# Kernel tuning notes

Hardware: AMD Instinct MI355X
Metric: run time of the kernel (lower is better)

## Reference

```python
import jax, jax.numpy as jnp
import numpy as np

# Mamba2 config fixed by MambaIndexer.__init__: d_state=64, expand=1, headdim=32
D_MODEL = 1024
D_STATE = 64
EXPAND = 1
D_INNER = EXPAND * D_MODEL          # 1024
HEADDIM = 32
NHEADS = D_INNER // HEADDIM         # 32
D_CONV = 4
NGROUPS = 1
IDX_DIM = 64
SEQ = 2048
CONV_DIM = D_INNER + 2 * NGROUPS * D_STATE            # 1152 (x, B, C share the conv)
D_IN_PROJ = 2 * D_INNER + 2 * NGROUPS * D_STATE + NHEADS  # 2208 (z, xBC, dt)


def setup_inputs() -> dict:
    key = jax.random.key(0)
    ks = jax.random.split(key, 10)
    s = 0.02  # init scale for projection weights
    return {
        "x": jax.random.normal(ks[0], (SEQ, D_MODEL), jnp.float32),
        "W_in": jax.random.normal(ks[1], (D_MODEL, D_IN_PROJ), jnp.float32) * s,
        "conv_w": jax.random.normal(ks[2], (CONV_DIM, D_CONV), jnp.float32) * s,
        "conv_b": jnp.zeros((CONV_DIM,), jnp.float32),
        "dt_bias": jax.random.normal(ks[3], (NHEADS,), jnp.float32) * 0.1,
        "A_log": jax.random.uniform(ks[4], (NHEADS,), jnp.float32, 0.0, 1.5),
        "D": jax.random.normal(ks[5], (NHEADS,), jnp.float32),
        "norm_w": jnp.ones((D_INNER,), jnp.float32),
        "W_out": jax.random.normal(ks[6], (D_INNER, D_MODEL), jnp.float32) * s,
        "Wq": jax.random.normal(ks[7], (D_MODEL, IDX_DIM), jnp.float32) * s,
        "Wk": jax.random.normal(ks[8], (D_MODEL, IDX_DIM), jnp.float32) * s,
    }


def _mamba2(x, W_in, conv_w, conv_b, dt_bias, A_log, D, norm_w, W_out):
    L = x.shape[0]
    zxbcdt = x @ W_in                                   # (L, 2208)
    z = zxbcdt[:, :D_INNER]                             # gate
    xBC = zxbcdt[:, D_INNER:D_INNER + CONV_DIM]
    dt = jax.nn.softplus(zxbcdt[:, D_INNER + CONV_DIM:] + dt_bias)  # (L, H)
    # causal depthwise conv1d over seq, kernel 4, then silu
    conv = jax.lax.conv_general_dilated(
        xBC.T[None],                                    # (1, C, L)
        conv_w[:, None, :],                             # (C, 1, K)
        (1,), [(D_CONV - 1, 0)], feature_group_count=CONV_DIM)
    xBC = jax.nn.silu(conv[0].T + conv_b)               # (L, C)
    xs = xBC[:, :D_INNER].reshape(L, NHEADS, HEADDIM)   # (L, H, P)
    B = xBC[:, D_INNER:D_INNER + D_STATE]               # (L, N), ngroups=1
    C = xBC[:, D_INNER + D_STATE:]                      # (L, N)
    A = -jnp.exp(A_log)                                 # (H,)
    dA = jnp.exp(dt * A)                                # (L, H)
    dBx = jnp.einsum('lh,lhp,ln->lhpn', dt, xs, B)      # (L, H, P, N)

    def step(h, inp):
        dA_t, dBx_t, C_t = inp
        h = dA_t[:, None, None] * h + dBx_t             # (H, P, N)
        return h, jnp.einsum('hpn,n->hp', h, C_t)

    h0 = jnp.zeros((NHEADS, HEADDIM, D_STATE), x.dtype)
    _, y = jax.lax.scan(step, h0, (dA, dBx, C))         # y: (L, H, P)
    y = y + D[:, None] * xs                             # skip connection
    y = y.reshape(L, D_INNER) * jax.nn.silu(z)          # gated
    y = y * jax.lax.rsqrt(jnp.mean(y * y, axis=-1, keepdims=True) + 1e-5) * norm_w
    return y @ W_out                                    # (L, d_model)


def reference(x, W_in, conv_w, conv_b, dt_bias, A_log, D, norm_w, W_out, Wq, Wk):
    L = x.shape[0]
    x_mamba = _mamba2(x, W_in, conv_w, conv_b, dt_bias, A_log, D, norm_w, W_out)
    q = x_mamba @ Wq                                    # (L, idx)
    k = x @ Wk                                          # (L, idx)
    scores = jnp.einsum('ti,si->ts', q, k) * (IDX_DIM ** -0.5)
    mask = jnp.tril(jnp.ones((L, L), dtype=bool))
    return jnp.where(mask, scores, -jnp.inf)
```

## Files before the change

### kernel.cpp

```cpp
#include <hip/hip_runtime.h>
#include <hip/hip_bf16.h>
#include <math.h>
#include <float.h>

#define SEQ 2048
#define DMODEL 1024
#define DINNER 1024
#define DSTATE 64
#define HEADDIM 32
#define NHEADS 32
#define DCONV 4
#define CONVDIM 1152
#define DINPROJ 2208
#define DINPROJ_PAD 2304
#define IDXDIM 64

#define CHUNK 64
#define NCHUNKS (SEQ / CHUNK)

#define MASK_VAL (-1e30f)

typedef unsigned short u16;
typedef __bf16 bf16x8 __attribute__((ext_vector_type(8)));
typedef float f32x4 __attribute__((ext_vector_type(4)));
typedef u16 u16x8 __attribute__((ext_vector_type(8)));

__device__ __forceinline__ u16 f2bf(float x) {
    unsigned int u = __float_as_uint(x);
    u += 0x7FFFu + ((u >> 16) & 1u);
    return (u16)(u >> 16);
}
__device__ __forceinline__ float bf2f(u16 u) {
    return __uint_as_float(((unsigned int)u) << 16);
}
__device__ __forceinline__ bf16x8 asbf(u16x8 v) {
    union { u16x8 u; bf16x8 b; } c; c.u = v; return c.b;
}

__device__ __forceinline__ void gload_lds16(const void* g, void* l) {
    __builtin_amdgcn_global_load_lds(
        (const __attribute__((address_space(1))) void*)g,
        (__attribute__((address_space(3))) void*)l, 16, 0, 0);
}

__global__ __launch_bounds__(256)
void convert_all(const float* __restrict__ x, u16* __restrict__ xb,
                 const float* __restrict__ W_in, u16* __restrict__ Wt_in,
                 const float* __restrict__ Wk, u16* __restrict__ Wt_k) {
    __shared__ float tile[32][33];
    int b = blockIdx.x, tid = threadIdx.x;

    if (b < 2048) {
        int i = (b * 256 + tid) * 4;
        float4 v = *(const float4*)(x + i);
        ushort4 o;
        o.x = f2bf(v.x); o.y = f2bf(v.y); o.z = f2bf(v.z); o.w = f2bf(v.w);
        *(ushort4*)(xb + i) = o;
        return;
    }
    const float* W; u16* Wt; int N, bx, by;
    if (b < 4352) { int l = b - 2048; W = W_in; Wt = Wt_in; N = DINPROJ; bx = l % 72; by = l / 72; }
    else          { int l = b - 4352; W = Wk;   Wt = Wt_k;  N = IDXDIM;  bx = l & 1;  by = l >> 1; }
    int k0 = by * 32, n0 = bx * 32;
    int tj = tid & 31, ti = tid >> 5;
#pragma unroll
    for (int s = 0; s < 4; s++) {
        int i = ti + s * 8;
        float v = 0.f;
        if (n0 + tj < N) v = W[(size_t)(k0 + i) * N + n0 + tj];
        tile[i][tj] = v;
    }
    __syncthreads();
#pragma unroll
    for (int s = 0; s < 4; s++) {
        int i = ti + s * 8;
        Wt[(size_t)(n0 + i) * DMODEL + k0 + tj] = f2bf(tile[tj][i]);
    }
}

template<int BM, int BN, int WM, int WN, bool OUT_BF16>
__device__ __forceinline__
void gemm_body(u16* As, u16* Bs,
               const u16* __restrict__ A, const u16* __restrict__ Bt,
               void* __restrict__ Cout, int N, int K, int bx, int by) {
    constexpr int BK = 64;
    constexpr int SLOTS = BK / 8;
    constexpr int MI = WM / 16, NI = WN / 16;
    constexpr int WCOLS = BN / WN;
    constexpr int A_ISS = (BM * BK * 2) / (256 * 16);
    constexpr int B_ISS = (BN * BK * 2) / (256 * 16);

    const int tid = threadIdx.x;
    const int lane = tid & 63;
    const int wid = tid >> 6;
    const int wbase = wid * 64;
    const int wr = wid / WCOLS, wc = wid % WCOLS;
    const int row0 = by * BM, col0 = bx * BN;

    f32x4 acc[MI][NI];
#pragma unroll
    for (int m = 0; m < MI; m++)
#pragma unroll
        for (int n = 0; n < NI; n++) acc[m][n] = (f32x4){0.f, 0.f, 0.f, 0.f};

    const int lrow = lane & 15, lkg = lane >> 4;

    for (int kb = 0; kb < K; kb += BK) {
#pragma unroll
        for (int i = 0; i < A_ISS; i++) {
            int e = (i * 256 + tid) * 8;
            int r = e / BK;
            int sl = (e >> 3) & (SLOTS - 1);
            int c = ((sl ^ (r & (SLOTS - 1))) << 3);
            gload_lds16(A + (size_t)(row0 + r) * K + kb + c,
                        &As[(i * 256 + wbase) * 8]);
        }
#pragma unroll
        for (int i = 0; i < B_ISS; i++) {
            int e = (i * 256 + tid) * 8;
            int r = e / BK;
            int sl = (e >> 3) & (SLOTS - 1);
            int c = ((sl ^ (r & (SLOTS - 1))) << 3);
            gload_lds16(Bt + (size_t)(col0 + r) * K + kb + c,
                        &Bs[(i * 256 + wbase) * 8]);
        }
        __syncthreads();

#pragma unroll
        for (int ks = 0; ks < BK / 32; ks++) {
            bf16x8 af[MI], bff[NI];
#pragma unroll
            for (int m = 0; m < MI; m++) {
                int row = wr * WM + m * 16 + lrow;
                int koff = ks * 32 + lkg * 8;
                af[m] = *(const bf16x8*)&As[row * BK + (koff ^ ((row & (SLOTS - 1)) << 3))];
            }
#pragma unroll
            for (int n = 0; n < NI; n++) {
                int row = wc * WN + n * 16 + lrow;
                int koff = ks * 32 + lkg * 8;
                bff[n] = *(const bf16x8*)&Bs[row * BK + (koff ^ ((row & (SLOTS - 1)) << 3))];
            }
#pragma unroll
            for (int m = 0; m < MI; m++)
#pragma unroll
                for (int n = 0; n < NI; n++)
                    acc[m][n] = __builtin_amdgcn_mfma_f32_16x16x32_bf16(
                        af[m], bff[n], acc[m][n], 0, 0, 0);
        }
        __syncthreads();
    }

    const int crow = (lane >> 4) * 4;
    const int ccol = lane & 15;
#pragma unroll
    for (int m = 0; m < MI; m++) {
#pragma unroll
        for (int n = 0; n < NI; n++) {
            int col = col0 + wc * WN + n * 16 + ccol;
            if (col < N) {
                size_t base = (size_t)(row0 + wr * WM + m * 16 + crow) * N + col;
#pragma unroll
                for (int r = 0; r < 4; r++) {
                    if (OUT_BF16)
                        ((u16*)Cout)[base + (size_t)r * N] = f2bf(acc[m][n][r]);
                    else
                        ((float*)Cout)[base + (size_t)r * N] = acc[m][n][r];
                }
            }
        }
    }
}

__global__ __launch_bounds__(256)
void gemm1_k(const u16* __restrict__ xb, const u16* __restrict__ Wt_in,
             u16* __restrict__ zx_bf, const u16* __restrict__ Wt_k,
             u16* __restrict__ kb,
             const float* __restrict__ Wq, const float* __restrict__ W_out,
             const float* __restrict__ norm_w, u16* __restrict__ Wt_nq) {
    extern __shared__ __align__(16) u16 sm[];
    int b = blockIdx.x, tid = threadIdx.x;
    if (b < 288) {
        gemm_body<128, 128, 64, 64, true>(sm, sm + 128 * 64, xb, Wt_in, zx_bf,
                                          DINPROJ, DMODEL, b % 18, b / 18);
        return;
    }
    if (b < 304) {
        gemm_body<128, 64, 64, 32, true>(sm, sm + 128 * 64, xb, Wt_k, kb,
                                         IDXDIM, DMODEL, 0, b - 288);
        return;
    }
    float* ftile = (float*)sm;
    u16* Bs = sm + 64 * 64 * 2;
    int d0 = (b - 304) * 64;
    int lane = tid & 63, wid = tid >> 6, lrow = lane & 15, lkg = lane >> 4;
    f32x4 acc[4];
#pragma unroll
    for (int ct = 0; ct < 4; ct++) acc[ct] = (f32x4){0.f, 0.f, 0.f, 0.f};

    for (int k0 = 0; k0 < DMODEL; k0 += 64) {
#pragma unroll
        for (int it = 0; it < 4; it++) {
            int e = it * 256 + tid;
            int r = e >> 4, c4 = e & 15;
            *(float4*)&ftile[r * 64 + c4 * 4] =
                *(const float4*)&Wq[(size_t)(k0 + r) * IDXDIM + c4 * 4];
        }
#pragma unroll
        for (int it = 0; it < 2; it++) {
            int e = it * 256 + tid;
            int d = e >> 3, sl = e & 7;
            const float* src = &W_out[(size_t)(d0 + d) * DMODEL + k0 + sl * 8];
            float4 v0 = *(const float4*)src, v1 = *(const float4*)(src + 4);
            u16x8 v;
            v[0] = f2bf(v0.x); v[1] = f2bf(v0.y); v[2] = f2bf(v0.z); v[3] = f2bf(v0.w);
            v[4] = f2bf(v1.x); v[5] = f2bf(v1.y); v[6] = f2bf(v1.z); v[7] = f2bf(v1.w);
            *(u16x8*)&Bs[d * 64 + ((sl ^ (d & 7)) << 3)] = v;
        }
        __syncthreads();
#pragma unroll
        for (int ks = 0; ks < 2; ks++) {
            int j = wid * 16 + lrow;
            int koff = ks * 32 + lkg * 8;
            u16x8 av;
#pragma unroll
            for (int kk = 0; kk < 8; kk++) av[kk] = f2bf(ftile[(koff + kk) * 64 + j]);
            bf16x8 a = asbf(av);
#pragma unroll
            for (int ct = 0; ct < 4; ct++) {
                int d = ct * 16 + lrow;
                bf16x8 bv = *(const bf16x8*)&Bs[d * 64 + (koff ^ ((d & 7) << 3))];
                acc[ct] = __builtin_amdgcn_mfma_f32_16x16x32_bf16(a, bv, acc[ct], 0, 0, 0);
            }
        }
        __syncthreads();
    }
    int ccol = lane & 15;
#pragma unroll
    for (int ct = 0; ct < 4; ct++)
#pragma unroll
        for (int r = 0; r < 4; r++) {
            int j = wid * 16 + lkg * 4 + r;
            int d = d0 + ct * 16 + ccol;
            Wt_nq[(size_t)j * DMODEL + d] = f2bf(acc[ct][r] * norm_w[d]);
        }
}

__global__ void conv_dt_kernel(const u16* __restrict__ zx_bf,
                               const float* __restrict__ conv_w,
                               const float* __restrict__ conv_b,
                               const float* __restrict__ dt_bias,
                               u16* __restrict__ xs_bf,
                               u16* __restrict__ B_bf,
                               u16* __restrict__ C_bf,
                               float* __restrict__ dt_out) {
    int b = blockIdx.x;
    if (b >= 9216) {
        int idx = (b - 9216) * 256 + threadIdx.x;
        int t = idx >> 5, h = idx & 31;
        float v = bf2f(zx_bf[(size_t)t * DINPROJ + (DINNER + CONVDIM) + h]) + dt_bias[h];
        dt_out[idx] = (v > 20.f) ? v : log1pf(expf(v));
        return;
    }
    int idx = b * 256 + threadIdx.x;
    int t = idx / CONVDIM, c = idx % CONVDIM;
    float4 w = *(const float4*)&conv_w[c * 4];
    const u16* src = zx_bf + DINNER + c;
    float acc = conv_b[c];
    float wj[4] = {w.x, w.y, w.z, w.w};
#pragma unroll
    for (int j = 0; j < 4; j++) {
        int tt = t - 3 + j;
        if (tt >= 0) acc += bf2f(src[(size_t)tt * DINPROJ]) * wj[j];
    }
    u16 rb = f2bf(acc / (1.f + expf(-acc)));
    if (c < DINNER) xs_bf[(size_t)t * DINNER + c] = rb;
    else if (c < DINNER + DSTATE) B_bf[(size_t)t * DSTATE + (c - DINNER)] = rb;
    else C_bf[(size_t)t * DSTATE + (c - DINNER - DSTATE)] = rb;
}

__global__ __launch_bounds__(256)
void ssd_state_kernel(const u16* __restrict__ xs_bf,
                      const u16* __restrict__ B_bf,
                      const float* __restrict__ dt,
                      const float* __restrict__ A_log,
                      float* __restrict__ S,
                      float* __restrict__ Pc) {
    int bid = blockIdx.x;
    int c = bid >> 5, h = bid & 31;
    int t0 = c * CHUNK;
    __shared__ __align__(16) u16 Xwt[HEADDIM * CHUNK];
    __shared__ __align__(16) u16 Bt[DSTATE * CHUNK];
    __shared__ float w_lds[CHUNK];
    int tid = threadIdx.x, lane = tid & 63;

    if (tid < 64) {
        float Ah = -__expf(A_log[h]);
        float dv = dt[(t0 + tid) * NHEADS + h];
        float sv = dv * Ah;
#pragma unroll
        for (int d = 1; d < 64; d <<= 1) {
            float o = __shfl_up(sv, d, 64);
            if (lane >= d) sv += o;
        }
        float s63 = __shfl(sv, 63, 64);
        w_lds[tid] = __expf(s63 - sv) * dv;
        if (tid == 63) Pc[c * NHEADS + h] = __expf(sv);
    }
    __syncthreads();

#pragma unroll
    for (int it = 0; it < 8; it++) {
        int e = it * 256 + tid;
        int j = e >> 5, p = e & 31;
        float xv = bf2f(xs_bf[(size_t)(t0 + j) * DINNER + h * HEADDIM + p]) * w_lds[j];
        Xwt[p * 64 + (j ^ ((p & 7) << 3))] = f2bf(xv);
    }
#pragma unroll
    for (int it = 0; it < 16; it++) {
        int e = it * 256 + tid;
        int j = e >> 6, n = e & 63;
        Bt[n * 64 + (j ^ ((n & 7) << 3))] = B_bf[(size_t)(t0 + j) * DSTATE + n];
    }
    __syncthreads();

    int wid = tid >> 6, lrow = lane & 15, lkg = lane >> 4;
    int rt = wid & 1, ctb = (wid >> 1) * 2;
    f32x4 acc[2];
    acc[0] = (f32x4){0.f, 0.f, 0.f, 0.f};
    acc[1] = (f32x4){0.f, 0.f, 0.f, 0.f};
#pragma unroll
    for (int ks = 0; ks < 2; ks++) {
        int p = rt * 16 + lrow;
        bf16x8 av = *(const bf16x8*)&Xwt[p * 64 + ((ks * 32 + lkg * 8) ^ ((p & 7) << 3))];
#pragma unroll
        for (int ci = 0; ci < 2; ci++) {
            int n = (ctb + ci) * 16 + lrow;
            bf16x8 bv = *(const bf16x8*)&Bt[n * 64 + ((ks * 32 + lkg * 8) ^ ((n & 7) << 3))];
            acc[ci] = __builtin_amdgcn_mfma_f32_16x16x32_bf16(av, bv, acc[ci], 0, 0, 0);
        }
    }
    size_t base = (size_t)c * 1024 + h * 32;
#pragma unroll
    for (int ci = 0; ci < 2; ci++)
#pragma unroll
        for (int r = 0; r < 4; r++) {
            int p = rt * 16 + lkg * 4 + r;
            int n = (ctb + ci) * 16 + lrow;
            S[(base + p) * 64 + n] = acc[ci][r];
        }
}

__global__ void state_scan_kernel(float* __restrict__ S,
                                  const float* __restrict__ Pc) {
    int gt = blockIdx.x * blockDim.x + threadIdx.x;
    int w = gt >> 6;
    int lane = gt & 63;
    int h = w >> 5;
    size_t off0 = (size_t)w * 64 + lane;
    float h_run = 0.f;
    float s_next = S[off0];
    float pc_next = Pc[h];
    for (int c = 0; c < NCHUNKS; c++) {
        float s = s_next, pc = pc_next;
        if (c < NCHUNKS - 1) {
            s_next = S[off0 + (size_t)(c + 1) * 65536];
            pc_next = Pc[(c + 1) * NHEADS + h];
        }
        S[off0 + (size_t)c * 65536] = h_run;
        h_run = h_run * pc + s;
    }
}

__global__ __launch_bounds__(256)
void ssd_y_kernel(const u16* __restrict__ xs_bf,
                  const u16* __restrict__ B_bf,
                  const u16* __restrict__ C_bf,
                  const float* __restrict__ dt,
                  const float* __restrict__ A_log,
                  const float* __restrict__ S,
                  const float* __restrict__ Dp,
                  u16* __restrict__ y_bf) {
    int bid = blockIdx.x;
    int c = bid >> 5, h = bid & 31;
    int t0 = c * CHUNK;
    __shared__ __align__(16) u16 Cbf[CHUNK * DSTATE];
    __shared__ __align__(16) u16 Bbf[CHUNK * DSTATE];
    __shared__ __align__(16) u16 Gs[CHUNK * CHUNK];
    __shared__ __align__(16) u16 aCbf[CHUNK * DSTATE];
    __shared__ __align__(16) u16 Xt[HEADDIM * CHUNK];
    __shared__ __align__(16) u16 H0s[HEADDIM * DSTATE];
    __shared__ float s_lds[64], dt_lds[64], a_lds[64];
    int tid = threadIdx.x, lane = tid & 63, wid = tid >> 6;

#pragma unroll
    for (int it = 0; it < 16; it++) {
        int e = it * 256 + tid;
        int i = e >> 6, n = e & 63;
        int nsw = n ^ ((i & 7) << 3);
        Bbf[i * 64 + nsw] = B_bf[(size_t)(t0 + i) * DSTATE + n];
        Cbf[i * 64 + nsw] = C_bf[(size_t)(t0 + i) * DSTATE + n];
    }
#pragma unroll
    for (int it = 0; it < 8; it++) {
        int e = it * 256 + tid;
        int j = e >> 5, p = e & 31;
        Xt[p * 64 + (j ^ ((p & 7) << 3))] =
            xs_bf[(size_t)(t0 + j) * DINNER + h * HEADDIM + p];
    }
#pragma unroll
    for (int it = 0; it < 8; it++) {
        int e = it * 256 + tid;
        int p = e >> 6, n = e & 63;
        H0s[p * 64 + (n ^ ((p & 7) << 3))] =
            f2bf(S[((size_t)c * 1024 + h * 32 + p) * 64 + n]);
    }
    if (tid < 64) {
        float Ah = -__expf(A_log[h]);
        float dv = dt[(t0 + tid) * NHEADS + h];
        float sv = dv * Ah;
#pragma unroll
        for (int d = 1; d < 64; d <<= 1) {
            float o = __shfl_up(sv, d, 64);
            if (lane >= d) sv += o;
        }
        s_lds[tid] = sv;
        dt_lds[tid] = dv;
        a_lds[tid] = __expf(sv);
    }
    __syncthreads();

    int lrow = lane & 15, lkg = lane >> 4;

    f32x4 g[4];
#pragma unroll
    for (int ct = 0; ct < 4; ct++) g[ct] = (f32x4){0.f, 0.f, 0.f, 0.f};
#pragma unroll
    for (int ks = 0; ks < 2; ks++) {
        int i = wid * 16 + lrow;
        bf16x8 af = *(const bf16x8*)&Cbf[i * 64 + ((ks * 32 + lkg * 8) ^ ((i & 7) << 3))];
#pragma unroll
        for (int ct = 0; ct < 4; ct++) {
            int j = ct * 16 + lrow;
            bf16x8 bv = *(const bf16x8*)&Bbf[j * 64 + ((ks * 32 + lkg * 8) ^ ((j & 7) << 3))];
            g[ct] = __builtin_amdgcn_mfma_f32_16x16x32_bf16(af, bv, g[ct], 0, 0, 0);
        }
    }
#pragma unroll
    for (int ct = 0; ct < 4; ct++) {
        int j = ct * 16 + lrow;
        float sj = s_lds[j], dtj = dt_lds[j];
#pragma unroll
        for (int r = 0; r < 4; r++) {
            int i = wid * 16 + lkg * 4 + r;
            float si = s_lds[i];
            float v = (j <= i) ? g[ct][r] * __expf(fminf(si - sj, 0.f)) * dtj : 0.f;
            Gs[i * 64 + (j ^ ((i & 7) << 3))] = f2bf(v);
        }
    }
#pragma unroll
    for (int it = 0; it < 16; it++) {
        int e = it * 256 + tid;
        int i = e >> 6, n = e & 63;
        int idx = i * 64 + (n ^ ((i & 7) << 3));
        aCbf[idx] = f2bf(a_lds[i] * bf2f(Cbf[idx]));
    }
    __syncthreads();

    f32x4 y[2];
    y[0] = (f32x4){0.f, 0.f, 0.f, 0.f};
    y[1] = (f32x4){0.f, 0.f, 0.f, 0.f};
#pragma unroll
    for (int ks = 0; ks < 2; ks++) {
        int i = wid * 16 + lrow;
        int koff = ks * 32 + lkg * 8;
        bf16x8 ga = *(const bf16x8*)&Gs[i * 64 + (koff ^ ((i & 7) << 3))];
        bf16x8 ca = *(const bf16x8*)&aCbf[i * 64 + (koff ^ ((i & 7) << 3))];
#pragma unroll
        for (int ct = 0; ct < 2; ct++) {
            int p = ct * 16 + lrow;
            bf16x8 xv = *(const bf16x8*)&Xt[p * 64 + (koff ^ ((p & 7) << 3))];
            y[ct] = __builtin_amdgcn_mfma_f32_16x16x32_bf16(ga, xv, y[ct], 0, 0, 0);
            bf16x8 hv = *(const bf16x8*)&H0s[p * 64 + (koff ^ ((p & 7) << 3))];
            y[ct] = __builtin_amdgcn_mfma_f32_16x16x32_bf16(ca, hv, y[ct], 0, 0, 0);
        }
    }
    float Dh = Dp[h];
#pragma unroll
    for (int ct = 0; ct < 2; ct++)
#pragma unroll
        for (int r = 0; r < 4; r++) {
            int i = wid * 16 + lkg * 4 + r;
            int p = ct * 16 + lrow;
            float xres = bf2f(Xt[p * 64 + (i ^ ((p & 7) << 3))]);
            y_bf[(size_t)(t0 + i) * DINNER + h * HEADDIM + p] = f2bf(y[ct][r] + Dh * xres);
        }
}

__global__ __launch_bounds__(256)
void rmsq_kernel(const u16* __restrict__ y_bf, const u16* __restrict__ zx_bf,
                 const u16* __restrict__ Wt_nq, u16* __restrict__ qb) {
    __shared__ __align__(16) u16 As[16 * 128];
    __shared__ __align__(16) u16 Bs[64 * 128];
    __shared__ float ssr[16];
    int t0 = blockIdx.x * 16;
    int tid = threadIdx.x, lane = tid & 63, wid = tid >> 6;
    int r = tid >> 4, sl = tid & 15;
    int lrow = lane & 15, lkg = lane >> 4;
    float ss = 0.f;
    f32x4 acc = (f32x4){0.f, 0.f, 0.f, 0.f};

    for (int kc = 0; kc < 8; kc++) {
        int k0 = kc * 128;
#pragma unroll
        for (int it = 0; it < 4; it++) {
            int e = it * 256 + tid;
            int rr = e >> 4, sl2 = e & 15;
            gload_lds16(Wt_nq + (size_t)rr * DMODEL + k0 + ((sl2 ^ (rr & 15)) << 3),
                        &Bs[(it * 256 + wid * 64) * 8]);
        }
        {
            int c0 = sl * 8;
            u16x8 yv = *(const u16x8*)&y_bf[(size_t)(t0 + r) * DINNER + k0 + c0];
            u16x8 zv = *(const u16x8*)&zx_bf[(size_t)(t0 + r) * DINPROJ + k0 + c0];
            u16x8 o;
#pragma unroll
            for (int i = 0; i < 8; i++) {
                float z = bf2f(zv[i]);
                float v = bf2f(yv[i]) * (z / (1.f + __expf(-z)));
                ss += v * v;
                o[i] = f2bf(v);
            }
            *(u16x8*)&As[r * 128 + ((sl ^ r) << 3)] = o;
        }
        __syncthreads();
#pragma unroll
        for (int ks = 0; ks < 4; ks++) {
            int koff = ks * 32 + lkg * 8;
            bf16x8 a = *(const bf16x8*)&As[lrow * 128 + (koff ^ (lrow << 3))];
            int rb = wid * 16 + lrow;
            bf16x8 bv = *(const bf16x8*)&Bs[rb * 128 + (koff ^ ((rb & 15) << 3))];
            acc = __builtin_amdgcn_mfma_f32_16x16x32_bf16(a, bv, acc, 0, 0, 0);
        }
        __syncthreads();
    }
    ss += __shfl_xor(ss, 1, 64);
    ss += __shfl_xor(ss, 2, 64);
    ss += __shfl_xor(ss, 4, 64);
    ss += __shfl_xor(ss, 8, 64);
    if (sl == 0) ssr[r] = ss;
    __syncthreads();
    int ccol = lane & 15;
#pragma unroll
    for (int rr = 0; rr < 4; rr++) {
        int row = lkg * 4 + rr;
        float scale = rsqrtf(ssr[row] / 1024.f + 1e-5f);
        qb[(size_t)(t0 + row) * IDXDIM + wid * 16 + ccol] = f2bf(acc[rr] * scale);
    }
}

__global__ __launch_bounds__(256)
void scores_kernel(const u16* __restrict__ q, const u16* __restrict__ k,
                   float* __restrict__ out) {
    int bx = blockIdx.x, by = blockIdx.y;
    int row0 = by * 64, col0 = bx * 64;
    int tid = threadIdx.x;
    if (bx > by) {
        float4 mv = make_float4(MASK_VAL, MASK_VAL, MASK_VAL, MASK_VAL);
#pragma unroll
        for (int it = 0; it < 4; it++) {
            int e = it * 256 + tid;
            int r = e >> 4, c4 = e & 15;
            *(float4*)&out[(size_t)(row0 + r) * SEQ + col0 + c4 * 4] = mv;
        }
        return;
    }
    __shared__ __align__(16) u16 qs[64 * 64];
    __shared__ __align__(16) u16 kss[64 * 64];
    int lane = tid & 63, wid = tid >> 6, lrow = lane & 15, lkg = lane >> 4;
#pragma unroll
    for (int it = 0; it < 2; it++) {
        int e = (it * 256 + tid) * 8;
        int r = e >> 6, c0 = e & 63;
        int csw = c0 ^ ((r & 7) << 3);
        *(u16x8*)&qs[r * 64 + csw] = *(const u16x8*)&q[(size_t)(row0 + r) * IDXDIM + c0];
        *(u16x8*)&kss[r * 64 + csw] = *(const u16x8*)&k[(size_t)(col0 + r) * IDXDIM + c0];
    }
    __syncthreads();
    f32x4 g[4];
#pragma unroll
    for (int ct = 0; ct < 4; ct++) g[ct] = (f32x4){0.f, 0.f, 0.f, 0.f};
#pragma unroll
    for (int ks = 0; ks < 2; ks++) {
        int i = wid * 16 + lrow;
        int koff = ks * 32 + lkg * 8;
        bf16x8 af = *(const bf16x8*)&qs[i * 64 + (koff ^ ((i & 7) << 3))];
#pragma unroll
        for (int ct = 0; ct < 4; ct++) {
            int j = ct * 16 + lrow;
            bf16x8 bv = *(const bf16x8*)&kss[j * 64 + (koff ^ ((j & 7) << 3))];
            g[ct] = __builtin_amdgcn_mfma_f32_16x16x32_bf16(af, bv, g[ct], 0, 0, 0);
        }
    }
#pragma unroll
    for (int ct = 0; ct < 4; ct++)
#pragma unroll
        for (int r = 0; r < 4; r++) {
            int trow = row0 + wid * 16 + lkg * 4 + r;
            int tcol = col0 + ct * 16 + lrow;
            out[(size_t)trow * SEQ + tcol] =
                (tcol <= trow) ? g[ct][r] * 0.125f : MASK_VAL;
        }
}

extern "C" void kernel_launch(void* const* d_in, const int* in_sizes, int n_in,
                              void* d_out, int out_size, void* d_ws, size_t ws_size,
                              hipStream_t stream) {
    const float* x       = (const float*)d_in[0];
    const float* W_in    = (const float*)d_in[1];
    const float* conv_w  = (const float*)d_in[2];
    const float* conv_b  = (const float*)d_in[3];
    const float* dt_bias = (const float*)d_in[4];
    const float* A_log   = (const float*)d_in[5];
    const float* Dp      = (const float*)d_in[6];
    const float* norm_w  = (const float*)d_in[7];
    const float* W_out   = (const float*)d_in[8];
    const float* Wq      = (const float*)d_in[9];
    const float* Wk      = (const float*)d_in[10];
    float* out = (float*)d_out;
    float* ws = (float*)d_ws;

    float* S  = ws;
    float* Pc = S + (size_t)SEQ * DINNER;
    float* dt = Pc + 1024;
    u16* ub = (u16*)(dt + SEQ * NHEADS);
    u16* zx_bf = ub;                 ub += (size_t)SEQ * DINPROJ;
    u16* y_bf  = ub;                 ub += (size_t)SEQ * DINNER;
    u16* xs_bf = ub;                 ub += (size_t)SEQ * DINNER;
    u16* B_bf  = ub;                 ub += SEQ * DSTATE;
    u16* C_bf  = ub;                 ub += SEQ * DSTATE;
    u16* qb    = ub;                 ub += SEQ * IDXDIM;
    u16* kb    = ub;                 ub += SEQ * IDXDIM;
    u16* xb    = ub;                 ub += (size_t)SEQ * DMODEL;
    u16* Wt_in = ub;                 ub += (size_t)DINPROJ_PAD * DMODEL;
    u16* Wt_k  = ub;                 ub += IDXDIM * DMODEL;
    u16* Wt_nq = ub;                 ub += IDXDIM * DMODEL;

    convert_all<<<4416, 256, 0, stream>>>(x, xb, W_in, Wt_in, Wk, Wt_k);

    gemm1_k<<<320, 256, 32768, stream>>>(xb, Wt_in, zx_bf, Wt_k, kb,
                                         Wq, W_out, norm_w, Wt_nq);

    conv_dt_kernel<<<9472, 256, 0, stream>>>(zx_bf, conv_w, conv_b, dt_bias,
                                             xs_bf, B_bf, C_bf, dt);

    ssd_state_kernel<<<NCHUNKS * NHEADS, 256, 0, stream>>>(xs_bf, B_bf, dt, A_log, S, Pc);
    state_scan_kernel<<<256, 256, 0, stream>>>(S, Pc);
    ssd_y_kernel<<<NCHUNKS * NHEADS, 256, 0, stream>>>(
        xs_bf, B_bf, C_bf, dt, A_log, S, Dp, y_bf);

    rmsq_kernel<<<SEQ / 16, 256, 0, stream>>>(y_bf, zx_bf, Wt_nq, qb);

    scores_kernel<<<dim3(SEQ / 64, SEQ / 64), 256, 0, stream>>>(qb, kb, out);
}
```

Baseline: 82.52 us.

## Run gemm1 with 512 threads per block and smaller per-wave tiles

Doubles the thread count of the first projection GEMM kernel from 256 to 512, so each block runs 8 wavefronts. Per-wave tiles shrink (64x32 instead of 64x64), and the cooperative LDS loads are rescaled to the new thread count. The Wq·W_out fused-weight path is remapped to a 2x4 wave grid. This raises latency hiding and occupancy within the 320-block grid, at the cost of less register-level reuse per wave and more LDS reads per MFMA.

```diff
diff --git a/kernel.cpp b/kernel.cpp
--- a/kernel.cpp
+++ b/kernel.cpp
@@ -78,7 +78,7 @@
     }
 }
 
-template<int BM, int BN, int WM, int WN, bool OUT_BF16>
+template<int NT, int BM, int BN, int WM, int WN, bool OUT_BF16>
 __device__ __forceinline__
 void gemm_body(u16* As, u16* Bs,
                const u16* __restrict__ A, const u16* __restrict__ Bt,
@@ -87,8 +87,8 @@
     constexpr int SLOTS = BK / 8;
     constexpr int MI = WM / 16, NI = WN / 16;
     constexpr int WCOLS = BN / WN;
-    constexpr int A_ISS = (BM * BK * 2) / (256 * 16);
-    constexpr int B_ISS = (BN * BK * 2) / (256 * 16);
+    constexpr int A_ISS = (BM * BK * 2) / (NT * 16);
+    constexpr int B_ISS = (BN * BK * 2) / (NT * 16);
 
     const int tid = threadIdx.x;
     const int lane = tid & 63;
@@ -108,21 +108,21 @@
     for (int kb = 0; kb < K; kb += BK) {
 #pragma unroll
         for (int i = 0; i < A_ISS; i++) {
-            int e = (i * 256 + tid) * 8;
+            int e = (i * NT + tid) * 8;
             int r = e / BK;
             int sl = (e >> 3) & (SLOTS - 1);
             int c = ((sl ^ (r & (SLOTS - 1))) << 3);
             gload_lds16(A + (size_t)(row0 + r) * K + kb + c,
-                        &As[(i * 256 + wbase) * 8]);
+                        &As[(i * NT + wbase) * 8]);
         }
 #pragma unroll
         for (int i = 0; i < B_ISS; i++) {
-            int e = (i * 256 + tid) * 8;
+            int e = (i * NT + tid) * 8;
             int r = e / BK;
             int sl = (e >> 3) & (SLOTS - 1);
             int c = ((sl ^ (r & (SLOTS - 1))) << 3);
             gload_lds16(Bt + (size_t)(col0 + r) * K + kb + c,
-                        &Bs[(i * 256 + wbase) * 8]);
+                        &Bs[(i * NT + wbase) * 8]);
         }
         __syncthreads();
 
@@ -172,7 +172,7 @@
     }
 }
 
-__global__ __launch_bounds__(256)
+__global__ __launch_bounds__(512)
 void gemm1_k(const u16* __restrict__ xb, const u16* __restrict__ Wt_in,
              u16* __restrict__ zx_bf, const u16* __restrict__ Wt_k,
              u16* __restrict__ kb,
@@ -181,35 +181,34 @@
     extern __shared__ __align__(16) u16 sm[];
     int b = blockIdx.x, tid = threadIdx.x;
     if (b < 288) {
-        gemm_body<128, 128, 64, 64, true>(sm, sm + 128 * 64, xb, Wt_in, zx_bf,
-                                          DINPROJ, DMODEL, b % 18, b / 18);
+        gemm_body<512, 128, 128, 64, 32, true>(sm, sm + 128 * 64, xb, Wt_in, zx_bf,
+                                               DINPROJ, DMODEL, b % 18, b / 18);
         return;
     }
     if (b < 304) {
-        gemm_body<128, 64, 64, 32, true>(sm, sm + 128 * 64, xb, Wt_k, kb,
-                                         IDXDIM, DMODEL, 0, b - 288);
+        gemm_body<512, 128, 64, 32, 32, true>(sm, sm + 128 * 64, xb, Wt_k, kb,
+                                              IDXDIM, DMODEL, 0, b - 288);
         return;
     }
     float* ftile = (float*)sm;
-    u16* Bs = sm + 64 * 64 * 2;
+    u16* Bs = sm + 8192;
     int d0 = (b - 304) * 64;
     int lane = tid & 63, wid = tid >> 6, lrow = lane & 15, lkg = lane >> 4;
-    f32x4 acc[4];
-#pragma unroll
-    for (int ct = 0; ct < 4; ct++) acc[ct] = (f32x4){0.f, 0.f, 0.f, 0.f};
+    int wr = wid >> 2, wc = wid & 3;
+    f32x4 acc[2];
+    acc[0] = (f32x4){0.f, 0.f, 0.f, 0.f};
+    acc[1] = (f32x4){0.f, 0.f, 0.f, 0.f};
 
     for (int k0 = 0; k0 < DMODEL; k0 += 64) {
 #pragma unroll
-        for (int it = 0; it < 4; it++) {
-            int e = it * 256 + tid;
+        for (int it = 0; it < 2; it++) {
+            int e = it * 512 + tid;
             int r = e >> 4, c4 = e & 15;
             *(float4*)&ftile[r * 64 + c4 * 4] =
                 *(const float4*)&Wq[(size_t)(k0 + r) * IDXDIM + c4 * 4];
         }
-#pragma unroll
-        for (int it = 0; it < 2; it++) {
-            int e = it * 256 + tid;
-            int d = e >> 3, sl = e & 7;
+        {
+            int d = tid >> 3, sl = tid & 7;
             const float* src = &W_out[(size_t)(d0 + d) * DMODEL + k0 + sl * 8];
             float4 v0 = *(const float4*)src, v1 = *(const float4*)(src + 4);
             u16x8 v;
@@ -220,29 +219,28 @@
         __syncthreads();
 #pragma unroll
         for (int ks = 0; ks < 2; ks++) {
-            int j = wid * 16 + lrow;
             int koff = ks * 32 + lkg * 8;
-            u16x8 av;
-#pragma unroll
-            for (int kk = 0; kk < 8; kk++) av[kk] = f2bf(ftile[(koff + kk) * 64 + j]);
-            bf16x8 a = asbf(av);
-#pragma unroll
-            for (int ct = 0; ct < 4; ct++) {
-                int d = ct * 16 + lrow;
-                bf16x8 bv = *(const bf16x8*)&Bs[d * 64 + (koff ^ ((d & 7) << 3))];
-                acc[ct] = __builtin_amdgcn_mfma_f32_16x16x32_bf16(a, bv, acc[ct], 0, 0, 0);
+            int d = wc * 16 + lrow;
+            bf16x8 bv = *(const bf16x8*)&Bs[d * 64 + (koff ^ ((d & 7) << 3))];
+#pragma unroll
+            for (int m = 0; m < 2; m++) {
+                int j = wr * 32 + m * 16 + lrow;
+                u16x8 av;
+#pragma unroll
+                for (int kk = 0; kk < 8; kk++) av[kk] = f2bf(ftile[(koff + kk) * 64 + j]);
+                acc[m] = __builtin_amdgcn_mfma_f32_16x16x32_bf16(asbf(av), bv, acc[m], 0, 0, 0);
             }
         }
         __syncthreads();
     }
     int ccol = lane & 15;
 #pragma unroll
-    for (int ct = 0; ct < 4; ct++)
+    for (int m = 0; m < 2; m++)
 #pragma unroll
         for (int r = 0; r < 4; r++) {
-            int j = wid * 16 + lkg * 4 + r;
-            int d = d0 + ct * 16 + ccol;
-            Wt_nq[(size_t)j * DMODEL + d] = f2bf(acc[ct][r] * norm_w[d]);
+            int j = wr * 32 + m * 16 + lkg * 4 + r;
+            int d = d0 + wc * 16 + ccol;
+            Wt_nq[(size_t)j * DMODEL + d] = f2bf(acc[m][r] * norm_w[d]);
         }
 }
 
@@ -648,7 +646,7 @@
 
     convert_all<<<4416, 256, 0, stream>>>(x, xb, W_in, Wt_in, Wk, Wt_k);
 
-    gemm1_k<<<320, 256, 32768, stream>>>(xb, Wt_in, zx_bf, Wt_k, kb,
+    gemm1_k<<<320, 512, 32768, stream>>>(xb, Wt_in, zx_bf, Wt_k, kb,
                                          Wq, W_out, norm_w, Wt_nq);
 
     conv_dt_kernel<<<9472, 256, 0, stream>>>(zx_bf, conv_w, conv_b, dt_bias,
```

New measurement: 87.43 us (median of 3 runs). 1.06x slower.
